# Optimization experiments

Hardware: AMD Instinct MI355X
Metric: run time of the kernel (lower is better)

The kernel has to match this reference:

```python
import jax, jax.numpy as jnp
import numpy as np
jax.config.update("jax_enable_x64", True)

B, C, N_IN, N_OUT, K = 128, 16, 64, 32, 4
EPS = 1e-12


def _funcm(X, fn):
    # symmetric matrix function f(X) = V diag(f(w)) V^T via eigendecomposition
    w, V = jnp.linalg.eigh(X)
    return jnp.einsum('...ij,...j,...kj->...ik', V, fn(w), V)


def setup_inputs() -> dict:
    key = jax.random.key(0)
    k1, k2, k3 = jax.random.split(key, 3)
    # SPD inputs per (batch, channel): M M^T / n + I
    M = jax.random.normal(k1, (B, C, N_IN, N_IN), dtype=jnp.float32)
    x = M @ jnp.swapaxes(M, -1, -2) / N_IN + jnp.eye(N_IN, dtype=jnp.float32)
    # K BiMap candidate-op weights with orthonormal rows (Stiefel), as in SPDNet
    A = jax.random.normal(k2, (K, N_IN, N_OUT), dtype=jnp.float32)
    Q, _ = jnp.linalg.qr(A)              # [K, N_IN, N_OUT] orthonormal columns
    Ws = jnp.swapaxes(Q, -1, -2)         # [K, N_OUT, N_IN]
    # architecture mixing weights (normalized, as DARTS softmax output would be)
    w = jax.random.uniform(k3, (K,), dtype=jnp.float32)
    weights = w / jnp.sum(w)
    return {"x": x, "weights": weights, "Ws": Ws}


def reference(x, weights, Ws):
    xd = x.astype(jnp.float64)
    Wd = Ws.astype(jnp.float64)
    wd = weights.astype(jnp.float64)
    # K candidate ops (BiMap): op_k(x)[b,c] = W_k x[b,c] W_k^T  -> s: [B,C,K,m,m]
    s = jnp.einsum('koi,bcij,kpj->bckop', Wd, xd, Wd)
    # weighted Riemannian (Karcher) barycenter over the K ops, per (b, c):
    # init at Euclidean weighted mean, then one Karcher step
    G0 = jnp.einsum('k,bckij->bcij', wd, s)                          # [B,C,m,m]
    Sq = _funcm(G0, jnp.sqrt)                                        # G0^{1/2}
    Si = _funcm(G0, lambda e: 1.0 / jnp.sqrt(jnp.clip(e, EPS)))      # G0^{-1/2}
    T = jnp.einsum('bcij,bckjl,bclm->bckim', Si, s, Si)              # congruence
    L = _funcm(T, lambda e: jnp.log(jnp.clip(e, EPS)))               # logm
    U = jnp.einsum('k,bckij->bcij', wd, L)                           # weighted tangent mean
    return jnp.einsum('bcij,bcjl,bclm->bcim', Sq, _funcm(U, jnp.exp), Sq)  # [B,C,m,m]
```

## Files before the change

### kernel.cpp

```cpp
#include <hip/hip_runtime.h>
#include <math.h>


#define NTH 256
#define LDA 33

#define WV_SYNC()                                         \
  do {                                                    \
    asm volatile("s_waitcnt lgkmcnt(0)" ::: "memory");    \
    __builtin_amdgcn_sched_barrier(0);                    \
  } while (0)

struct SM {
  double W4[4][32 * LDA];
  double V4[4][32 * LDA];
  double Si[32 * LDA];
  double ew4[4][32];
};

__device__ inline void mm_nn_wave(double* __restrict__ D, const double* __restrict__ A,
                                  const double* __restrict__ B, int lane) {
  const int j = lane & 31, hi = lane >> 5;
  double cb[32];
#pragma unroll
  for (int m = 0; m < 32; ++m) cb[m] = B[m * LDA + j];
#pragma unroll 4
  for (int t = 0; t < 16; ++t) {
    const int i = 2 * t + hi;
    double acc = 0.0;
#pragma unroll
    for (int m = 0; m < 32; ++m) acc = fma(A[i * LDA + m], cb[m], acc);
    D[i * LDA + j] = acc;
  }
}

__device__ inline void mm_nn_blk(double* __restrict__ D, const double* __restrict__ A,
                                 const double* __restrict__ B, int tid) {
  const int j = tid & 31;
  double cb[32];
#pragma unroll
  for (int m = 0; m < 32; ++m) cb[m] = B[m * LDA + j];
#pragma unroll
  for (int t = 0; t < 4; ++t) {
    const int i = 8 * t + (tid >> 5);
    double acc = 0.0;
#pragma unroll
    for (int m = 0; m < 32; ++m) acc = fma(A[i * LDA + m], cb[m], acc);
    D[i * LDA + j] = acc;
  }
}

__device__ void eigh_onesided(const double* __restrict__ A, double* __restrict__ V,
                              double* __restrict__ ewv, int lane) {
  const int j = lane & 31, h = lane >> 5;
  double b[16], w[16];
#pragma unroll
  for (int i = 0; i < 16; ++i) {
    b[i] = A[(h * 16 + i) * LDA + j];
    w[i] = (h * 16 + i == j) ? 1.0 : 0.0;
  }
  for (int sweep = 0; sweep < 12; ++sweep) {
    bool any_rot = false;
    for (int m = 1; m < 32; ++m) {
      const int pj = j ^ m;
      double on2 = 0.0;
#pragma unroll
      for (int i = 0; i < 16; ++i) on2 = fma(b[i], b[i], on2);
      on2 += __shfl_xor(on2, 32, 64);
      double tp[16];
#pragma unroll
      for (int i = 0; i < 16; ++i) tp[i] = __shfl_xor(b[i], m, 64);
      double cr = 0.0;
#pragma unroll
      for (int i = 0; i < 16; ++i) cr = fma(b[i], tp[i], cr);
      cr += __shfl_xor(cr, 32, 64);
      const double op2 = __shfl_xor(on2, m, 64);
      if (cr * cr > 1e-18 * on2 * op2) {
        any_rot = true;
        const double gpp = (j < pj) ? on2 : op2;
        const double gqq = (j < pj) ? op2 : on2;
        const double tau = (gqq - gpp) / (2.0 * cr);
        const double t = ((tau >= 0.0) ? 1.0 : -1.0) /
                         (fabs(tau) + sqrt(1.0 + tau * tau));
        const double c = 1.0 / sqrt(1.0 + t * t);
        const double s = t * c;
        const double ss = (j < pj) ? -s : s;
#pragma unroll
        for (int i = 0; i < 16; ++i) b[i] = fma(ss, tp[i], c * b[i]);
#pragma unroll
        for (int i = 0; i < 16; ++i) tp[i] = __shfl_xor(w[i], m, 64);
#pragma unroll
        for (int i = 0; i < 16; ++i) w[i] = fma(ss, tp[i], c * w[i]);
      }
    }
    if (!__any(any_rot)) break;
  }
  double lam = 0.0;
#pragma unroll
  for (int i = 0; i < 16; ++i) lam = fma(b[i], w[i], lam);
  lam += __shfl_xor(lam, 32, 64);
#pragma unroll
  for (int i = 0; i < 16; ++i) V[(h * 16 + i) * LDA + j] = w[i];
  if (h == 0) ewv[j] = lam;
  WV_SYNC();
}

__global__ __launch_bounds__(NTH, 2) void mixedop_kernel(
    const float* __restrict__ xg, const float* __restrict__ wg,
    const float* __restrict__ Wg, float* __restrict__ outg,
    float* __restrict__ ws_s, double* __restrict__ ws_sq) {
  __shared__ SM sm;
  const int bc = blockIdx.x;
  const int tid = threadIdx.x;
  const int lane = tid & 63;
  const int wv = tid >> 6;

  char* base = (char*)&sm.W4[0][0];
  float* Xs = (float*)base;
  double* Ys = (double*)(base + 16640);
  float* Wst = (float*)(base + 33280);
  double* G0 = (double*)(base + 41600);

  for (int idx = tid; idx < 1056; idx += NTH) G0[idx] = 0.0;
  const float* xsrc = xg + (size_t)bc * 4096;
  for (int idx = tid; idx < 4096; idx += NTH)
    Xs[(idx >> 6) * 65 + (idx & 63)] = xsrc[idx];
  __syncthreads();

  for (int k = 0; k < 4; ++k) {
    const float* wsrc = Wg + k * 2048;
    for (int idx = tid; idx < 2048; idx += NTH)
      Wst[(idx >> 6) * 65 + (idx & 63)] = wsrc[idx];
    __syncthreads();
    {
      const int j = tid & 63;
      float cx[64];
#pragma unroll
      for (int m = 0; m < 64; ++m) cx[m] = Xs[m * 65 + j];
#pragma unroll
      for (int t = 0; t < 8; ++t) {
        const int o = 4 * t + (tid >> 6);
        double acc = 0.0;
#pragma unroll
        for (int m = 0; m < 64; ++m)
          acc = fma((double)Wst[o * 65 + m], (double)cx[m], acc);
        Ys[o * 65 + j] = acc;
      }
    }
    __syncthreads();
    {
      const double wkk = (double)wg[k];
      const int p = tid & 31;
      float cw[64];
#pragma unroll
      for (int m = 0; m < 64; ++m) cw[m] = Wst[p * 65 + m];
#pragma unroll
      for (int t = 0; t < 4; ++t) {
        const int o = 8 * t + (tid >> 5);
        double acc = 0.0;
#pragma unroll
        for (int m = 0; m < 64; ++m)
          acc = fma(Ys[o * 65 + m], (double)cw[m], acc);
        const int e = o * 32 + p;
        ws_s[(size_t)bc * 4096 + k * 1024 + e] = (float)acc;
        G0[o * LDA + p] += wkk * acc;
      }
    }
    __syncthreads();
  }

  for (int idx = tid; idx < 1024; idx += NTH) {
    const int i = idx >> 5, j = idx & 31;
    sm.W4[0][i * LDA + j] = G0[i * LDA + j];
  }
  __syncthreads();
  if (wv == 0) eigh_onesided(sm.W4[0], sm.V4[0], sm.ew4[0], lane);
  __syncthreads();
  {
    const int j = tid & 31;
    const double lam = sm.ew4[0][j];
    const double sq = sqrt(fmax(lam, 0.0));
    const double isq = 1.0 / sqrt(fmax(lam, 1e-12));
#pragma unroll
    for (int t = 0; t < 4; ++t) {
      const int i = 8 * t + (tid >> 5);
      const double v = sm.V4[0][i * LDA + j];
      sm.W4[1][i * LDA + j] = v * sq;
      sm.W4[2][i * LDA + j] = v * isq;
    }
  }
  __syncthreads();
  {
    const int j = tid & 31;
    double cb[32];
#pragma unroll
    for (int m = 0; m < 32; ++m) cb[m] = sm.V4[0][j * LDA + m];
#pragma unroll
    for (int t = 0; t < 4; ++t) {
      const int i = 8 * t + (tid >> 5);
      double a1 = 0.0, a2 = 0.0;
#pragma unroll
      for (int m = 0; m < 32; ++m) {
        a1 = fma(sm.W4[1][i * LDA + m], cb[m], a1);
        a2 = fma(sm.W4[2][i * LDA + m], cb[m], a2);
      }
      ws_sq[(size_t)bc * 1024 + i * 32 + j] = a1;
      sm.Si[i * LDA + j] = a2;
    }
  }
  __syncthreads();

  {
    const int k = wv;
    double* Ak = sm.W4[k];
    double* Vk = sm.V4[k];
    for (int t = 0; t < 16; ++t) {
      const int e = t * 64 + lane;
      Ak[(e >> 5) * LDA + (e & 31)] =
          (double)ws_s[(size_t)bc * 4096 + k * 1024 + e];
    }
    WV_SYNC();
    mm_nn_wave(Vk, sm.Si, Ak, lane);
    WV_SYNC();
    mm_nn_wave(Ak, Vk, sm.Si, lane);
    WV_SYNC();
    eigh_onesided(Ak, Vk, sm.ew4[k], lane);
    {
      const int j = lane & 31, hi = lane >> 5;
      const double lgl = log(fmax(sm.ew4[k][j], 1e-12));
#pragma unroll
      for (int t = 0; t < 16; ++t) {
        const int i = 2 * t + hi;
        Ak[i * LDA + j] = Vk[i * LDA + j] * lgl;
      }
    }
    WV_SYNC();
    {
      const double wkk = (double)wg[k];
      const int j = lane & 31, hi = lane >> 5;
      double cb[32];
#pragma unroll
      for (int m = 0; m < 32; ++m) cb[m] = Vk[j * LDA + m];
      double accv[16];
#pragma unroll
      for (int t = 0; t < 16; ++t) {
        const int i = 2 * t + hi;
        double a = 0.0;
#pragma unroll
        for (int m = 0; m < 32; ++m) a = fma(Ak[i * LDA + m], cb[m], a);
        accv[t] = wkk * a;
      }
      WV_SYNC();
#pragma unroll
      for (int t = 0; t < 16; ++t) Ak[(2 * t + hi) * LDA + j] = accv[t];
    }
  }
  __syncthreads();

  for (int idx = tid; idx < 1024; idx += NTH) {
    const int i = idx >> 5, j = idx & 31;
    sm.V4[1][i * LDA + j] = sm.W4[0][i * LDA + j] + sm.W4[1][i * LDA + j] +
                            sm.W4[2][i * LDA + j] + sm.W4[3][i * LDA + j];
  }
  __syncthreads();
  if (wv == 0) eigh_onesided(sm.V4[1], sm.V4[0], sm.ew4[0], lane);
  __syncthreads();
  {
    const int j = tid & 31;
    const double ex = exp(sm.ew4[0][j]);
#pragma unroll
    for (int t = 0; t < 4; ++t) {
      const int i = 8 * t + (tid >> 5);
      sm.V4[2][i * LDA + j] = sm.V4[0][i * LDA + j] * ex;
    }
  }
  __syncthreads();
  {
    const int j = tid & 31;
    double cb[32];
#pragma unroll
    for (int m = 0; m < 32; ++m) cb[m] = sm.V4[0][j * LDA + m];
#pragma unroll
    for (int t = 0; t < 4; ++t) {
      const int i = 8 * t + (tid >> 5);
      double acc = 0.0;
#pragma unroll
      for (int m = 0; m < 32; ++m) acc = fma(sm.V4[2][i * LDA + m], cb[m], acc);
      sm.V4[3][i * LDA + j] = acc;
    }
  }
  __syncthreads();
  for (int idx = tid; idx < 1024; idx += NTH)
    sm.W4[0][(idx >> 5) * LDA + (idx & 31)] = ws_sq[(size_t)bc * 1024 + idx];
  __syncthreads();
  mm_nn_blk(sm.W4[1], sm.W4[0], sm.V4[3], tid);
  __syncthreads();
  {
    const int j = tid & 31;
    double cb[32];
#pragma unroll
    for (int m = 0; m < 32; ++m) cb[m] = sm.W4[0][m * LDA + j];
#pragma unroll
    for (int t = 0; t < 4; ++t) {
      const int i = 8 * t + (tid >> 5);
      double acc = 0.0;
#pragma unroll
      for (int m = 0; m < 32; ++m)
        acc = fma(sm.W4[1][i * LDA + m], cb[m], acc);
      outg[(size_t)bc * 1024 + i * 32 + j] = (float)acc;
    }
  }
}

extern "C" void kernel_launch(void* const* d_in, const int* in_sizes, int n_in,
                              void* d_out, int out_size, void* d_ws, size_t ws_size,
                              hipStream_t stream) {
  const float* x = (const float*)d_in[0];
  const float* w = (const float*)d_in[1];
  const float* Ws = (const float*)d_in[2];
  float* out = (float*)d_out;

  const int nbc = in_sizes[0] / 4096;
  float* ws_s = (float*)d_ws;
  double* ws_sq = (double*)((char*)d_ws + (size_t)nbc * 4096 * sizeof(float));

  mixedop_kernel<<<dim3(nbc), dim3(NTH), 0, stream>>>(x, w, Ws, out, ws_s, ws_sq);
}
```

Baseline: 3.468 ms.

## Update column norms incrementally and use fast reciprocal/rsqrt in Jacobi eigensolver

Column squared norms in the one-sided Jacobi eigensolver are now computed once per sweep and updated analytically after each rotation (on2 ± t*cr), instead of being recomputed from 16 FMAs plus a cross-half shuffle for every pair. Double-precision divides and square roots in the rotation-angle calculation are replaced by float-seeded Newton-refined reciprocal and rsqrt. Dot products are split into four independent accumulators to shorten FMA dependency chains. The incremental norm update can drift numerically over a sweep and change the convergence behaviour.

```diff
diff --git a/kernel.cpp b/kernel.cpp
--- a/kernel.cpp
+++ b/kernel.cpp
@@ -18,6 +18,19 @@
   double ew4[4][32];
 };
 
+__device__ inline double fast_rcp(double x) {
+  double r = (double)(1.0f / (float)x);
+  r = r * (2.0 - x * r);
+  r = r * (2.0 - x * r);
+  return r;
+}
+__device__ inline double fast_rsqrt(double x) {
+  double r = (double)rsqrtf((float)x);
+  r = r * (1.5 - 0.5 * x * r * r);
+  r = r * (1.5 - 0.5 * x * r * r);
+  return r;
+}
+
 __device__ inline void mm_nn_wave(double* __restrict__ D, const double* __restrict__ A,
                                   const double* __restrict__ B, int lane) {
   const int j = lane & 31, hi = lane >> 5;
@@ -60,29 +73,44 @@
     w[i] = (h * 16 + i == j) ? 1.0 : 0.0;
   }
   for (int sweep = 0; sweep < 12; ++sweep) {
+    double n0 = 0.0, n1 = 0.0, n2 = 0.0, n3 = 0.0;
+#pragma unroll
+    for (int i = 0; i < 16; i += 4) {
+      n0 = fma(b[i + 0], b[i + 0], n0);
+      n1 = fma(b[i + 1], b[i + 1], n1);
+      n2 = fma(b[i + 2], b[i + 2], n2);
+      n3 = fma(b[i + 3], b[i + 3], n3);
+    }
+    double on2 = (n0 + n1) + (n2 + n3);
+    on2 += __shfl_xor(on2, 32, 64);
+
     bool any_rot = false;
     for (int m = 1; m < 32; ++m) {
       const int pj = j ^ m;
-      double on2 = 0.0;
-#pragma unroll
-      for (int i = 0; i < 16; ++i) on2 = fma(b[i], b[i], on2);
-      on2 += __shfl_xor(on2, 32, 64);
       double tp[16];
 #pragma unroll
       for (int i = 0; i < 16; ++i) tp[i] = __shfl_xor(b[i], m, 64);
-      double cr = 0.0;
-#pragma unroll
-      for (int i = 0; i < 16; ++i) cr = fma(b[i], tp[i], cr);
+      double c0 = 0.0, c1 = 0.0, c2 = 0.0, c3 = 0.0;
+#pragma unroll
+      for (int i = 0; i < 16; i += 4) {
+        c0 = fma(b[i + 0], tp[i + 0], c0);
+        c1 = fma(b[i + 1], tp[i + 1], c1);
+        c2 = fma(b[i + 2], tp[i + 2], c2);
+        c3 = fma(b[i + 3], tp[i + 3], c3);
+      }
+      double cr = (c0 + c1) + (c2 + c3);
       cr += __shfl_xor(cr, 32, 64);
       const double op2 = __shfl_xor(on2, m, 64);
       if (cr * cr > 1e-18 * on2 * op2) {
         any_rot = true;
         const double gpp = (j < pj) ? on2 : op2;
         const double gqq = (j < pj) ? op2 : on2;
-        const double tau = (gqq - gpp) / (2.0 * cr);
-        const double t = ((tau >= 0.0) ? 1.0 : -1.0) /
-                         (fabs(tau) + sqrt(1.0 + tau * tau));
-        const double c = 1.0 / sqrt(1.0 + t * t);
+        const double tau = (gqq - gpp) * fast_rcp(2.0 * cr);
+        const double yt = 1.0 + tau * tau;
+        const double rs = fast_rsqrt(yt);
+        const double den = fabs(tau) + yt * rs;
+        const double t = ((tau >= 0.0) ? 1.0 : -1.0) * fast_rcp(den);
+        const double c = fast_rsqrt(1.0 + t * t);
         const double s = t * c;
         const double ss = (j < pj) ? -s : s;
 #pragma unroll
@@ -91,13 +119,20 @@
         for (int i = 0; i < 16; ++i) tp[i] = __shfl_xor(w[i], m, 64);
 #pragma unroll
         for (int i = 0; i < 16; ++i) w[i] = fma(ss, tp[i], c * w[i]);
+        on2 = (j < pj) ? fma(-t, cr, on2) : fma(t, cr, on2);
       }
     }
     if (!__any(any_rot)) break;
   }
-  double lam = 0.0;
-#pragma unroll
-  for (int i = 0; i < 16; ++i) lam = fma(b[i], w[i], lam);
+  double l0 = 0.0, l1 = 0.0, l2 = 0.0, l3 = 0.0;
+#pragma unroll
+  for (int i = 0; i < 16; i += 4) {
+    l0 = fma(b[i + 0], w[i + 0], l0);
+    l1 = fma(b[i + 1], w[i + 1], l1);
+    l2 = fma(b[i + 2], w[i + 2], l2);
+    l3 = fma(b[i + 3], w[i + 3], l3);
+  }
+  double lam = (l0 + l1) + (l2 + l3);
   lam += __shfl_xor(lam, 32, 64);
 #pragma unroll
   for (int i = 0; i < 16; ++i) V[(h * 16 + i) * LDA + j] = w[i];
```

Result: faster. 3.282 ms (-5.4%).
